# Kernel optimization log

Hardware: AMD Instinct MI355X
Metric: run time of the kernel (lower is better)

## Reference

```python
import jax, jax.numpy as jnp
import numpy as np

GLYPH_DIM = 4096
PADDING_IDX = GLYPH_DIM  # 4096
GLYPH_EMB = 20           # CHAR_EMB 16 + COLOR_EMB 4
HIDDEN = 32
MAX_LEN = 64


def setup_inputs() -> dict:
    key = jax.random.key(0)
    k1, k2, k3, k4, k5, k6, k7 = jax.random.split(key, 7)
    B, H, W = 8192, 21, 79
    glyph_chars = jax.random.randint(k1, (B, H, W), 0, 256, dtype=jnp.int32)
    glyph_colors = jax.random.randint(k2, (B, H, W), 0, 16, dtype=jnp.int32)
    # Embedding table with zero padding row (torch padding_idx semantics)
    emb_table = jax.random.normal(k3, (GLYPH_DIM + 1, GLYPH_EMB), dtype=jnp.float32) * 0.02
    emb_table = emb_table.at[PADDING_IDX].set(0.0)
    s = 1.0 / np.sqrt(HIDDEN)
    W_ih = jax.random.uniform(k4, (HIDDEN, GLYPH_EMB), minval=-s, maxval=s, dtype=jnp.float32)
    W_hh = jax.random.uniform(k5, (HIDDEN, HIDDEN), minval=-s, maxval=s, dtype=jnp.float32)
    b_ih = jax.random.uniform(k6, (HIDDEN,), minval=-s, maxval=s, dtype=jnp.float32)
    b_hh = jax.random.uniform(k7, (HIDDEN,), minval=-s, maxval=s, dtype=jnp.float32)
    return {"glyph_chars": glyph_chars, "glyph_colors": glyph_colors,
            "emb_table": emb_table, "W_ih": W_ih, "W_hh": W_hh,
            "b_ih": b_ih, "b_hh": b_hh}


def _encode_bag(glyph_chars, glyph_colors):
    """Batched sorted-unique compaction over the bounded glyph id range."""
    B = glyph_chars.shape[0]
    g_ids = ((glyph_chars << 4) + glyph_colors).reshape(B, -1)  # [B, H*W]
    # presence[b, g] = glyph g appears in sample b (batched histogram)
    bidx = jnp.broadcast_to(jnp.arange(B, dtype=g_ids.dtype)[:, None], g_ids.shape)
    presence = jnp.zeros((B, GLYPH_DIM), dtype=bool).at[bidx, g_ids].set(True)
    # compact: present ids keep their value, absent become PADDING_IDX (=4096),
    # so sorting yields ascending unique ids followed by padding.
    ids = jnp.arange(GLYPH_DIM, dtype=jnp.int32)
    keys = jnp.where(presence, ids, jnp.int32(PADDING_IDX))
    bag = jnp.sort(keys, axis=1)[:, :MAX_LEN]  # [B, MAX_LEN]
    lengths = jnp.minimum(presence.sum(axis=1), MAX_LEN)  # [B]
    return bag, lengths


def reference(glyph_chars, glyph_colors, emb_table, W_ih, W_hh, b_ih, b_hh):
    bag, lengths = _encode_bag(glyph_chars, glyph_colors)
    emb = emb_table[bag]  # [B, MAX_LEN, GLYPH_EMB]
    B = emb.shape[0]

    # packed RNN == plain RNN where hidden state freezes past each sequence length
    xs = jnp.swapaxes(emb, 0, 1)  # [T, B, E]

    def step(h, inp):
        xt, t = inp
        h_new = jnp.tanh(xt @ W_ih.T + b_ih + h @ W_hh.T + b_hh)
        h = jnp.where((t < lengths)[:, None], h_new, h)
        return h, None

    h0 = jnp.zeros((B, HIDDEN), dtype=emb.dtype)
    h, _ = jax.lax.scan(step, h0, (xs, jnp.arange(MAX_LEN)))
    return (h, emb, bag)
```

## Files before the change

### kernel.cpp

```cpp
#include <hip/hip_runtime.h>

#define HW 1659
#define PADID 4096
#define EMB 20
#define HID 32
#define MAXLEN 64

typedef float v2f __attribute__((ext_vector_type(2)));

template <int CTRL>
__device__ __forceinline__ float dppf(float v) {
    return __builtin_bit_cast(float,
        __builtin_amdgcn_update_dpp(0, __builtin_bit_cast(int, v),
                                    CTRL, 0xF, 0xF, true));
}
#define DPP_XOR1 0xB1
#define DPP_XOR2 0x4E
#define DPP_XOR7 0x141
#define DPP_XORF 0x140

__global__ __launch_bounds__(128) void proj_kernel(
    const float* __restrict__ emb_table, const float* __restrict__ W_ih,
    float* __restrict__ proj)
{
    const int tid = threadIdx.x;
    const int g = blockIdx.x * 4 + (tid >> 5);
    const int j = tid & 31;
    if (g > PADID) return;
    const float* er = emb_table + (size_t)g * EMB;
    const float* wr = W_ih + j * EMB;
    float s = 0.f;
#pragma unroll
    for (int k = 0; k < EMB; k++) s += wr[k] * er[k];
    proj[(size_t)g * HID + j] = s;
}

__global__ __launch_bounds__(256) void bag_emb_kernel(
    const int* __restrict__ chars, const int* __restrict__ colors,
    const float* __restrict__ emb_table,
    float* __restrict__ out_emb, float* __restrict__ out_bag)
{
    __shared__ unsigned char pres[4096];
    __shared__ int bagl[64];
    __shared__ int wsum[4];

    const int b   = blockIdx.x;
    const int tid = threadIdx.x;
    const int lane = tid & 63;
    const int wv   = tid >> 6;

    const int base = b * HW;
    const int pe = (4 - (base & 3)) & 3;
    const int nv = (HW - pe) >> 2;
    const int nt = HW - pe - (nv << 2);
    const int4* c4 = (const int4*)(chars + base + pe);
    const int4* k4 = (const int4*)(colors + base + pe);

    int4 ca = c4[tid], ka = k4[tid];
    const bool has2 = (tid + 256) < nv;
    const int i2 = has2 ? tid + 256 : tid;
    int4 cb = c4[i2], kb = k4[i2];
    int gp = -1, gt = -1;
    if (tid < pe) gp = (chars[base + tid] << 4) + colors[base + tid];
    if (tid < nt) {
        int i = base + pe + (nv << 2) + tid;
        gt = (chars[i] << 4) + colors[i];
    }

    ((uint4*)pres)[tid] = make_uint4(0u, 0u, 0u, 0u);
    if (tid < 64) bagl[tid] = PADID;
    __syncthreads();

    pres[(ca.x << 4) + ka.x] = 1;
    pres[(ca.y << 4) + ka.y] = 1;
    pres[(ca.z << 4) + ka.z] = 1;
    pres[(ca.w << 4) + ka.w] = 1;
    if (has2) {
        pres[(cb.x << 4) + kb.x] = 1;
        pres[(cb.y << 4) + kb.y] = 1;
        pres[(cb.z << 4) + kb.z] = 1;
        pres[(cb.w << 4) + kb.w] = 1;
    }
    if (gp >= 0) pres[gp] = 1;
    if (gt >= 0) pres[gt] = 1;
    __syncthreads();

    uint4 w4 = ((const uint4*)pres)[tid];
    const unsigned M = 0x01010101u;
    int cnt = __popc(w4.x & M) + __popc(w4.y & M)
            + __popc(w4.z & M) + __popc(w4.w & M);

    int pre = cnt;
#pragma unroll
    for (int d = 1; d < 64; d <<= 1) {
        int v = __shfl_up(pre, d, 64);
        if (lane >= d) pre += v;
    }
    if (lane == 63) wsum[wv] = pre;
    __syncthreads();
    int wbase = 0;
#pragma unroll
    for (int w2 = 0; w2 < 4; w2++) wbase += (w2 < wv) ? wsum[w2] : 0;
    int p = wbase + pre - cnt;

    unsigned wrd[4] = {w4.x, w4.y, w4.z, w4.w};
#pragma unroll
    for (int c = 0; c < 4; c++) {
#pragma unroll
        for (int k = 0; k < 4; k++) {
            if ((wrd[c] >> (8 * k)) & 1) {
                if (p < 64) bagl[p] = 16 * tid + 4 * c + k;
                p++;
            }
        }
    }
    __syncthreads();

    if (tid < 64) out_bag[(size_t)b * 64 + tid] = (float)bagl[tid];

    const float4* tab4 = (const float4*)emb_table;
    float4* dst4 = (float4*)(out_emb + (size_t)b * (MAXLEN * EMB));
    for (int q = tid; q < MAXLEN * 5; q += 256) {
        int t = q / 5;
        int m = q - t * 5;
        int row = bagl[t];
        dst4[q] = tab4[row * 5 + m];
    }
}

__global__ __launch_bounds__(128, 2) void rnn_kernel(
    const float* __restrict__ proj, const float* __restrict__ bagf,
    const float* __restrict__ W_hh,
    const float* __restrict__ b_ih, const float* __restrict__ b_hh,
    float* __restrict__ out_h)
{
    const int tid  = threadIdx.x;
    const int wv   = tid >> 6;
    const int lane = tid & 63;
    const int sl   = lane >> 4;
    const int ib   = wv * 4 + sl;
    const int jj   = lane & 15;
    const int b    = blockIdx.x * 8 + ib;

    const int GMAP[16] = {0,1,2,3, 7,6,5,4, 15,14,13,12,11,10,9,8};

    v2f w0[16], w1[16];
    const float2* wr0 = (const float2*)(W_hh + (2 * jj) * HID);
    const float2* wr1 = (const float2*)(W_hh + (2 * jj + 1) * HID);
#pragma unroll
    for (int m = 0; m < 16; m++) {
        const int c = jj ^ GMAP[m];
        float2 a = wr0[c], bb = wr1[c];
        w0[m] = (v2f){a.x, a.y};
        w1[m] = (v2f){bb.x, bb.y};
    }
    const float sb0 = b_ih[2 * jj]     + b_hh[2 * jj];
    const float sb1 = b_ih[2 * jj + 1] + b_hh[2 * jj + 1];

    const float* bps = bagf + (size_t)b * 64;

    unsigned long long mm0 = __ballot(bps[jj]      < 4095.5f);
    unsigned long long mm1 = __ballot(bps[jj + 16] < 4095.5f);
    unsigned long long mm2 = __ballot(bps[jj + 32] < 4095.5f);
    unsigned long long mm3 = __ballot(bps[jj + 48] < 4095.5f);
    const int sh = sl * 16;
    const int len = __popc((unsigned)((mm0 >> sh) & 0xFFFFu))
                  + __popc((unsigned)((mm1 >> sh) & 0xFFFFu))
                  + __popc((unsigned)((mm2 >> sh) & 0xFFFFu))
                  + __popc((unsigned)((mm3 >> sh) & 0xFFFFu));

    int idxC = (int)bps[1];
    float2 pv = ((const float2*)(proj + (size_t)((int)bps[0]) * HID))[jj];

    float h0 = 0.f, h1 = 0.f;
    for (int t = 0; t < MAXLEN; t++) {
        const int t2 = (t + 2 < MAXLEN) ? (t + 2) : (MAXLEN - 1);
        const int idxD = (int)bps[t2];
        const float2 pvn = ((const float2*)(proj + (size_t)idxC * HID))[jj];

        v2f g[16];
        g[0] = (v2f){h0, h1};
        g[1] = (v2f){dppf<DPP_XOR1>(g[0].x), dppf<DPP_XOR1>(g[0].y)};
        g[2] = (v2f){dppf<DPP_XOR2>(g[0].x), dppf<DPP_XOR2>(g[0].y)};
        g[3] = (v2f){dppf<DPP_XOR2>(g[1].x), dppf<DPP_XOR2>(g[1].y)};
#pragma unroll
        for (int m = 0; m < 4; m++)
            g[4 + m] = (v2f){dppf<DPP_XOR7>(g[m].x), dppf<DPP_XOR7>(g[m].y)};
#pragma unroll
        for (int m = 0; m < 8; m++)
            g[8 + m] = (v2f){dppf<DPP_XORF>(g[m].x), dppf<DPP_XORF>(g[m].y)};

        v2f a0 = (v2f){0.f, 0.f}, b0 = a0, a1 = a0, b1 = a0;
#pragma unroll
        for (int m = 0; m < 16; m += 2) {
            a0 = __builtin_elementwise_fma(w0[m],     g[m],     a0);
            b0 = __builtin_elementwise_fma(w0[m + 1], g[m + 1], b0);
            a1 = __builtin_elementwise_fma(w1[m],     g[m],     a1);
            b1 = __builtin_elementwise_fma(w1[m + 1], g[m + 1], b1);
        }
        float s0 = sb0 + pv.x + (a0.x + a0.y) + (b0.x + b0.y);
        float s1 = sb1 + pv.y + (a1.x + a1.y) + (b1.x + b1.y);

        float e0 = __expf(2.f * s0);
        float e1 = __expf(2.f * s1);
        float th0 = 1.f - 2.f * __builtin_amdgcn_rcpf(e0 + 1.f);
        float th1 = 1.f - 2.f * __builtin_amdgcn_rcpf(e1 + 1.f);

        h0 = (t < len) ? th0 : h0;
        h1 = (t < len) ? th1 : h1;

        pv = pvn; idxC = idxD;
    }

    ((float2*)(out_h + (size_t)b * HID))[jj] = make_float2(h0, h1);
}

__global__ __launch_bounds__(128, 4) void rnn_kernel_noproj(
    const float* __restrict__ emb, const float* __restrict__ bagf,
    const float* __restrict__ W_ih, const float* __restrict__ W_hh,
    const float* __restrict__ b_ih, const float* __restrict__ b_hh,
    float* __restrict__ out_h)
{
    __shared__ float hbuf[4][32];
    const int tid = threadIdx.x;
    const int ib  = tid >> 5;
    const int j   = tid & 31;
    const int b   = blockIdx.x * 4 + ib;

    float wih[EMB];
#pragma unroll
    for (int k = 0; k < EMB; k++) wih[k] = W_ih[j * EMB + k];
    float whh[HID];
#pragma unroll
    for (int k = 0; k < HID; k++) whh[k] = W_hh[j * HID + k];
    const float sbias = b_ih[j] + b_hh[j];

    const float* bp = bagf + (size_t)b * 64;
    unsigned long long m0 = __ballot(bp[j]      < 4095.5f);
    unsigned long long m1 = __ballot(bp[32 + j] < 4095.5f);
    const int half = ib & 1;
    const int len = __popc((unsigned)(m0 >> (half * 32)))
                  + __popc((unsigned)(m1 >> (half * 32)));

    hbuf[ib][j] = 0.f;
    asm volatile("s_waitcnt lgkmcnt(0)" ::: "memory");

    float h = 0.f;
    const float* xb = emb + (size_t)b * (MAXLEN * EMB);
    for (int t = 0; t < MAXLEN; t++) {
        const float4* xp = (const float4*)(xb + t * EMB);
        float4 x0 = xp[0], x1 = xp[1], x2 = xp[2], x3 = xp[3], x4 = xp[4];
        float s = sbias;
        const float4* hb4 = (const float4*)hbuf[ib];
#pragma unroll
        for (int m = 0; m < 8; m++) {
            float4 hv = hb4[m];
            s += whh[4*m+0]*hv.x + whh[4*m+1]*hv.y
               + whh[4*m+2]*hv.z + whh[4*m+3]*hv.w;
        }
        s += wih[0]*x0.x + wih[1]*x0.y + wih[2]*x0.z + wih[3]*x0.w;
        s += wih[4]*x1.x + wih[5]*x1.y + wih[6]*x1.z + wih[7]*x1.w;
        s += wih[8]*x2.x + wih[9]*x2.y + wih[10]*x2.z + wih[11]*x2.w;
        s += wih[12]*x3.x + wih[13]*x3.y + wih[14]*x3.z + wih[15]*x3.w;
        s += wih[16]*x4.x + wih[17]*x4.y + wih[18]*x4.z + wih[19]*x4.w;
        s = fminf(fmaxf(s, -9.f), 9.f);
        float e = __expf(2.f * s);
        float th = (e - 1.f) * __builtin_amdgcn_rcpf(e + 1.f);
        h = (t < len) ? th : h;
        hbuf[ib][j] = h;
        asm volatile("s_waitcnt lgkmcnt(0)" ::: "memory");
    }
    out_h[(size_t)b * HID + j] = h;
}

extern "C" void kernel_launch(void* const* d_in, const int* in_sizes, int n_in,
                              void* d_out, int out_size, void* d_ws, size_t ws_size,
                              hipStream_t stream) {
    const int*   chars     = (const int*)d_in[0];
    const int*   colors    = (const int*)d_in[1];
    const float* emb_table = (const float*)d_in[2];
    const float* W_ih      = (const float*)d_in[3];
    const float* W_hh      = (const float*)d_in[4];
    const float* b_ih      = (const float*)d_in[5];
    const float* b_hh      = (const float*)d_in[6];

    const int B = in_sizes[0] / HW;

    float* out     = (float*)d_out;
    float* out_h   = out;
    float* out_emb = out + (size_t)B * HID;
    float* out_bag = out_emb + (size_t)B * MAXLEN * EMB;

    const size_t proj_bytes = (size_t)(PADID + 1) * HID * sizeof(float);

    bag_emb_kernel<<<B, 256, 0, stream>>>(chars, colors, emb_table, out_emb, out_bag);

    if (ws_size >= proj_bytes) {
        float* proj = (float*)d_ws;
        proj_kernel<<<(PADID + 1 + 3) / 4, 128, 0, stream>>>(emb_table, W_ih, proj);
        rnn_kernel<<<B / 8, 128, 0, stream>>>(proj, out_bag, W_hh, b_ih, b_hh, out_h);
    } else {
        rnn_kernel_noproj<<<B / 4, 128, 0, stream>>>(out_emb, out_bag, W_ih, W_hh,
                                                     b_ih, b_hh, out_h);
    }
}
```

Measured before the change: 183.0 us.

## Process two samples per block in bag kernel, overlapping second sample's loads

The bag/embedding kernel now handles two batch samples per block. The second sample's chars and colors loads are issued before the first sample's scan and compaction, and the presence buffer is cleared and reused. This aims to hide global load latency and amortize block setup, at the cost of more registers and extra barriers, plus half as many blocks. It assumes B is even.

```diff
diff --git a/kernel.cpp b/kernel.cpp
--- a/kernel.cpp
+++ b/kernel.cpp
@@ -41,55 +41,72 @@
     float* __restrict__ out_emb, float* __restrict__ out_bag)
 {
     __shared__ unsigned char pres[4096];
-    __shared__ int bagl[64];
+    __shared__ int bagl[2][64];
     __shared__ int wsum[4];
 
-    const int b   = blockIdx.x;
-    const int tid = threadIdx.x;
+    const int tid  = threadIdx.x;
     const int lane = tid & 63;
     const int wv   = tid >> 6;
-
-    const int base = b * HW;
-    const int pe = (4 - (base & 3)) & 3;
-    const int nv = (HW - pe) >> 2;
-    const int nt = HW - pe - (nv << 2);
-    const int4* c4 = (const int4*)(chars + base + pe);
-    const int4* k4 = (const int4*)(colors + base + pe);
-
-    int4 ca = c4[tid], ka = k4[tid];
-    const bool has2 = (tid + 256) < nv;
-    const int i2 = has2 ? tid + 256 : tid;
-    int4 cb = c4[i2], kb = k4[i2];
-    int gp = -1, gt = -1;
-    if (tid < pe) gp = (chars[base + tid] << 4) + colors[base + tid];
-    if (tid < nt) {
-        int i = base + pe + (nv << 2) + tid;
-        gt = (chars[i] << 4) + colors[i];
+    const int b0   = blockIdx.x * 2;
+
+    const int base0 = b0 * HW;
+    const int pe0 = (4 - (base0 & 3)) & 3;
+    const int nv0 = (HW - pe0) >> 2;
+    const int nt0 = HW - pe0 - (nv0 << 2);
+    const int4* c40 = (const int4*)(chars + base0 + pe0);
+    const int4* k40 = (const int4*)(colors + base0 + pe0);
+    int4 ca0 = c40[tid], ka0 = k40[tid];
+    const bool h20 = (tid + 256) < nv0;
+    const int i20 = h20 ? tid + 256 : tid;
+    int4 cb0 = c40[i20], kb0 = k40[i20];
+    int gp0 = -1, gt0 = -1;
+    if (tid < pe0) gp0 = (chars[base0 + tid] << 4) + colors[base0 + tid];
+    if (tid < nt0) {
+        int i = base0 + pe0 + (nv0 << 2) + tid;
+        gt0 = (chars[i] << 4) + colors[i];
     }
 
     ((uint4*)pres)[tid] = make_uint4(0u, 0u, 0u, 0u);
-    if (tid < 64) bagl[tid] = PADID;
-    __syncthreads();
-
-    pres[(ca.x << 4) + ka.x] = 1;
-    pres[(ca.y << 4) + ka.y] = 1;
-    pres[(ca.z << 4) + ka.z] = 1;
-    pres[(ca.w << 4) + ka.w] = 1;
-    if (has2) {
-        pres[(cb.x << 4) + kb.x] = 1;
-        pres[(cb.y << 4) + kb.y] = 1;
-        pres[(cb.z << 4) + kb.z] = 1;
-        pres[(cb.w << 4) + kb.w] = 1;
-    }
-    if (gp >= 0) pres[gp] = 1;
-    if (gt >= 0) pres[gt] = 1;
-    __syncthreads();
+    if (tid < 128) ((int*)bagl)[tid] = PADID;
+    __syncthreads();
+
+    pres[(ca0.x << 4) + ka0.x] = 1;
+    pres[(ca0.y << 4) + ka0.y] = 1;
+    pres[(ca0.z << 4) + ka0.z] = 1;
+    pres[(ca0.w << 4) + ka0.w] = 1;
+    if (h20) {
+        pres[(cb0.x << 4) + kb0.x] = 1;
+        pres[(cb0.y << 4) + kb0.y] = 1;
+        pres[(cb0.z << 4) + kb0.z] = 1;
+        pres[(cb0.w << 4) + kb0.w] = 1;
+    }
+    if (gp0 >= 0) pres[gp0] = 1;
+    if (gt0 >= 0) pres[gt0] = 1;
+
+    const int base1 = base0 + HW;
+    const int pe1 = (4 - (base1 & 3)) & 3;
+    const int nv1 = (HW - pe1) >> 2;
+    const int nt1 = HW - pe1 - (nv1 << 2);
+    const int4* c41 = (const int4*)(chars + base1 + pe1);
+    const int4* k41 = (const int4*)(colors + base1 + pe1);
+    int4 ca1 = c41[tid], ka1 = k41[tid];
+    const bool h21 = (tid + 256) < nv1;
+    const int i21 = h21 ? tid + 256 : tid;
+    int4 cb1 = c41[i21], kb1 = k41[i21];
+    int gp1 = -1, gt1 = -1;
+    if (tid < pe1) gp1 = (chars[base1 + tid] << 4) + colors[base1 + tid];
+    if (tid < nt1) {
+        int i = base1 + pe1 + (nv1 << 2) + tid;
+        gt1 = (chars[i] << 4) + colors[i];
+    }
+    __syncthreads();
+
+    const unsigned M = 0x01010101u;
 
     uint4 w4 = ((const uint4*)pres)[tid];
-    const unsigned M = 0x01010101u;
+    ((uint4*)pres)[tid] = make_uint4(0u, 0u, 0u, 0u);
     int cnt = __popc(w4.x & M) + __popc(w4.y & M)
             + __popc(w4.z & M) + __popc(w4.w & M);
-
     int pre = cnt;
 #pragma unroll
     for (int d = 1; d < 64; d <<= 1) {
@@ -102,29 +119,86 @@
 #pragma unroll
     for (int w2 = 0; w2 < 4; w2++) wbase += (w2 < wv) ? wsum[w2] : 0;
     int p = wbase + pre - cnt;
-
-    unsigned wrd[4] = {w4.x, w4.y, w4.z, w4.w};
-#pragma unroll
-    for (int c = 0; c < 4; c++) {
-#pragma unroll
-        for (int k = 0; k < 4; k++) {
-            if ((wrd[c] >> (8 * k)) & 1) {
-                if (p < 64) bagl[p] = 16 * tid + 4 * c + k;
-                p++;
+    {
+        unsigned wrd[4] = {w4.x, w4.y, w4.z, w4.w};
+#pragma unroll
+        for (int c = 0; c < 4; c++) {
+#pragma unroll
+            for (int k = 0; k < 4; k++) {
+                if ((wrd[c] >> (8 * k)) & 1) {
+                    if (p < 64) bagl[0][p] = 16 * tid + 4 * c + k;
+                    p++;
+                }
             }
         }
     }
     __syncthreads();
 
-    if (tid < 64) out_bag[(size_t)b * 64 + tid] = (float)bagl[tid];
-
+    pres[(ca1.x << 4) + ka1.x] = 1;
+    pres[(ca1.y << 4) + ka1.y] = 1;
+    pres[(ca1.z << 4) + ka1.z] = 1;
+    pres[(ca1.w << 4) + ka1.w] = 1;
+    if (h21) {
+        pres[(cb1.x << 4) + kb1.x] = 1;
+        pres[(cb1.y << 4) + kb1.y] = 1;
+        pres[(cb1.z << 4) + kb1.z] = 1;
+        pres[(cb1.w << 4) + kb1.w] = 1;
+    }
+    if (gp1 >= 0) pres[gp1] = 1;
+    if (gt1 >= 0) pres[gt1] = 1;
+
+    if (tid < 64) out_bag[(size_t)b0 * 64 + tid] = (float)bagl[0][tid];
     const float4* tab4 = (const float4*)emb_table;
-    float4* dst4 = (float4*)(out_emb + (size_t)b * (MAXLEN * EMB));
-    for (int q = tid; q < MAXLEN * 5; q += 256) {
-        int t = q / 5;
-        int m = q - t * 5;
-        int row = bagl[t];
-        dst4[q] = tab4[row * 5 + m];
+    {
+        float4* dst4 = (float4*)(out_emb + (size_t)b0 * (MAXLEN * EMB));
+        for (int q = tid; q < MAXLEN * 5; q += 256) {
+            int t = q / 5;
+            int m = q - t * 5;
+            int row = bagl[0][t];
+            dst4[q] = tab4[row * 5 + m];
+        }
+    }
+    __syncthreads();
+
+    uint4 w4b = ((const uint4*)pres)[tid];
+    int cntb = __popc(w4b.x & M) + __popc(w4b.y & M)
+             + __popc(w4b.z & M) + __popc(w4b.w & M);
+    int preb = cntb;
+#pragma unroll
+    for (int d = 1; d < 64; d <<= 1) {
+        int v = __shfl_up(preb, d, 64);
+        if (lane >= d) preb += v;
+    }
+    if (lane == 63) wsum[wv] = preb;
+    __syncthreads();
+    int wbaseb = 0;
+#pragma unroll
+    for (int w2 = 0; w2 < 4; w2++) wbaseb += (w2 < wv) ? wsum[w2] : 0;
+    int pb = wbaseb + preb - cntb;
+    {
+        unsigned wrd[4] = {w4b.x, w4b.y, w4b.z, w4b.w};
+#pragma unroll
+        for (int c = 0; c < 4; c++) {
+#pragma unroll
+            for (int k = 0; k < 4; k++) {
+                if ((wrd[c] >> (8 * k)) & 1) {
+                    if (pb < 64) bagl[1][pb] = 16 * tid + 4 * c + k;
+                    pb++;
+                }
+            }
+        }
+    }
+    __syncthreads();
+
+    if (tid < 64) out_bag[(size_t)(b0 + 1) * 64 + tid] = (float)bagl[1][tid];
+    {
+        float4* dst4 = (float4*)(out_emb + (size_t)(b0 + 1) * (MAXLEN * EMB));
+        for (int q = tid; q < MAXLEN * 5; q += 256) {
+            int t = q / 5;
+            int m = q - t * 5;
+            int row = bagl[1][t];
+            dst4[q] = tab4[row * 5 + m];
+        }
     }
 }
 
@@ -293,7 +367,7 @@
 
     const size_t proj_bytes = (size_t)(PADID + 1) * HID * sizeof(float);
 
-    bag_emb_kernel<<<B, 256, 0, stream>>>(chars, colors, emb_table, out_emb, out_bag);
+    bag_emb_kernel<<<B / 2, 256, 0, stream>>>(chars, colors, emb_table, out_emb, out_bag);
 
     if (ws_size >= proj_bytes) {
         float* proj = (float*)d_ws;
```

After: 190.0 us. 3.8% more time.

## Batch-prefetch projected inputs in two 32-step halves and fully unroll RNN loop

Applied to the files above, without the earlier changes.

The RNN kernel now loads all 32 bag indices and their projected input rows into registers up front for each half of the sequence, instead of prefetching one step two iterations ahead. Both 32-step halves are fully unrolled, and the length is computed from the loaded indices rather than with ballots. The aim is to issue all gather loads at once so their latency overlaps, taking memory latency off the serial recurrence. This raises register pressure, since 64 extra VGPRs are held for pvA/pvB, so occupancy is pinned with waves_per_eu(2,2).

```diff
diff --git a/kernel.cpp b/kernel.cpp
--- a/kernel.cpp
+++ b/kernel.cpp
@@ -128,7 +128,9 @@
     }
 }
 
-__global__ __launch_bounds__(128, 2) void rnn_kernel(
+__global__ __launch_bounds__(128)
+__attribute__((amdgpu_waves_per_eu(2, 2)))
+void rnn_kernel(
     const float* __restrict__ proj, const float* __restrict__ bagf,
     const float* __restrict__ W_hh,
     const float* __restrict__ b_ih, const float* __restrict__ b_hh,
@@ -158,26 +160,25 @@
     const float sb1 = b_ih[2 * jj + 1] + b_hh[2 * jj + 1];
 
     const float* bps = bagf + (size_t)b * 64;
-
-    unsigned long long mm0 = __ballot(bps[jj]      < 4095.5f);
-    unsigned long long mm1 = __ballot(bps[jj + 16] < 4095.5f);
-    unsigned long long mm2 = __ballot(bps[jj + 32] < 4095.5f);
-    unsigned long long mm3 = __ballot(bps[jj + 48] < 4095.5f);
-    const int sh = sl * 16;
-    const int len = __popc((unsigned)((mm0 >> sh) & 0xFFFFu))
-                  + __popc((unsigned)((mm1 >> sh) & 0xFFFFu))
-                  + __popc((unsigned)((mm2 >> sh) & 0xFFFFu))
-                  + __popc((unsigned)((mm3 >> sh) & 0xFFFFu));
-
-    int idxC = (int)bps[1];
-    float2 pv = ((const float2*)(proj + (size_t)((int)bps[0]) * HID))[jj];
+    const float2* proj2 = (const float2*)proj;
+
+    float2 pvA[32];
+    int lenA = 0;
+    {
+        int idx[32];
+#pragma unroll
+        for (int t = 0; t < 32; t++) idx[t] = (int)bps[t];
+#pragma unroll
+        for (int t = 0; t < 32; t++) {
+            lenA += (idx[t] < PADID) ? 1 : 0;
+            pvA[t] = proj2[idx[t] * 16 + jj];
+        }
+    }
 
     float h0 = 0.f, h1 = 0.f;
-    for (int t = 0; t < MAXLEN; t++) {
-        const int t2 = (t + 2 < MAXLEN) ? (t + 2) : (MAXLEN - 1);
-        const int idxD = (int)bps[t2];
-        const float2 pvn = ((const float2*)(proj + (size_t)idxC * HID))[jj];
-
+
+#pragma unroll
+    for (int t = 0; t < 32; t++) {
         v2f g[16];
         g[0] = (v2f){h0, h1};
         g[1] = (v2f){dppf<DPP_XOR1>(g[0].x), dppf<DPP_XOR1>(g[0].y)};
@@ -198,18 +199,65 @@
             a1 = __builtin_elementwise_fma(w1[m],     g[m],     a1);
             b1 = __builtin_elementwise_fma(w1[m + 1], g[m + 1], b1);
         }
-        float s0 = sb0 + pv.x + (a0.x + a0.y) + (b0.x + b0.y);
-        float s1 = sb1 + pv.y + (a1.x + a1.y) + (b1.x + b1.y);
+        float s0 = sb0 + pvA[t].x + (a0.x + a0.y) + (b0.x + b0.y);
+        float s1 = sb1 + pvA[t].y + (a1.x + a1.y) + (b1.x + b1.y);
 
         float e0 = __expf(2.f * s0);
         float e1 = __expf(2.f * s1);
         float th0 = 1.f - 2.f * __builtin_amdgcn_rcpf(e0 + 1.f);
         float th1 = 1.f - 2.f * __builtin_amdgcn_rcpf(e1 + 1.f);
 
+        h0 = (t < lenA) ? th0 : h0;
+        h1 = (t < lenA) ? th1 : h1;
+    }
+
+    float2 pvB[32];
+    int lenB = 0;
+    {
+        int idx[32];
+#pragma unroll
+        for (int t = 0; t < 32; t++) idx[t] = (int)bps[32 + t];
+#pragma unroll
+        for (int t = 0; t < 32; t++) {
+            lenB += (idx[t] < PADID) ? 1 : 0;
+            pvB[t] = proj2[idx[t] * 16 + jj];
+        }
+    }
+    const int len = lenA + lenB;
+
+#pragma unroll
+    for (int t2 = 0; t2 < 32; t2++) {
+        const int t = 32 + t2;
+        v2f g[16];
+        g[0] = (v2f){h0, h1};
+        g[1] = (v2f){dppf<DPP_XOR1>(g[0].x), dppf<DPP_XOR1>(g[0].y)};
+        g[2] = (v2f){dppf<DPP_XOR2>(g[0].x), dppf<DPP_XOR2>(g[0].y)};
+        g[3] = (v2f){dppf<DPP_XOR2>(g[1].x), dppf<DPP_XOR2>(g[1].y)};
+#pragma unroll
+        for (int m = 0; m < 4; m++)
+            g[4 + m] = (v2f){dppf<DPP_XOR7>(g[m].x), dppf<DPP_XOR7>(g[m].y)};
+#pragma unroll
+        for (int m = 0; m < 8; m++)
+            g[8 + m] = (v2f){dppf<DPP_XORF>(g[m].x), dppf<DPP_XORF>(g[m].y)};
+
+        v2f a0 = (v2f){0.f, 0.f}, b0 = a0, a1 = a0, b1 = a0;
+#pragma unroll
+        for (int m = 0; m < 16; m += 2) {
+            a0 = __builtin_elementwise_fma(w0[m],     g[m],     a0);
+            b0 = __builtin_elementwise_fma(w0[m + 1], g[m + 1], b0);
+            a1 = __builtin_elementwise_fma(w1[m],     g[m],     a1);
+            b1 = __builtin_elementwise_fma(w1[m + 1], g[m + 1], b1);
+        }
+        float s0 = sb0 + pvB[t2].x + (a0.x + a0.y) + (b0.x + b0.y);
+        float s1 = sb1 + pvB[t2].y + (a1.x + a1.y) + (b1.x + b1.y);
+
+        float e0 = __expf(2.f * s0);
+        float e1 = __expf(2.f * s1);
+        float th0 = 1.f - 2.f * __builtin_amdgcn_rcpf(e0 + 1.f);
+        float th1 = 1.f - 2.f * __builtin_amdgcn_rcpf(e1 + 1.f);
+
         h0 = (t < len) ? th0 : h0;
         h1 = (t < len) ? th1 : h1;
-
-        pv = pvn; idxC = idxD;
     }
 
     ((float2*)(out_h + (size_t)b * HID))[jj] = make_float2(h0, h1);
```

After: 181.2 us. About the same (-1.0%).

## Batch projection gathers in chunks of 16 steps and unroll RNN loop fully

Applied to the files above, without the earlier changes.

The RNN loop is restructured into four fully unrolled chunks. Each chunk first loads 16 bag indices and issues all 16 projection gathers, then runs the 16 recurrent steps. This replaces the depth-2 software prefetch with deeper memory-level parallelism. The ballot/popcount length computation is dropped in favour of a per-step padding test on the index, and occupancy is pinned to 2 waves per EU. The cost is higher register pressure from 16 buffered float2 values and indices, plus larger code.

```diff
diff --git a/kernel.cpp b/kernel.cpp
--- a/kernel.cpp
+++ b/kernel.cpp
@@ -128,7 +128,9 @@
     }
 }
 
-__global__ __launch_bounds__(128, 2) void rnn_kernel(
+__global__ __launch_bounds__(128)
+__attribute__((amdgpu_waves_per_eu(2, 2)))
+void rnn_kernel(
     const float* __restrict__ proj, const float* __restrict__ bagf,
     const float* __restrict__ W_hh,
     const float* __restrict__ b_ih, const float* __restrict__ b_hh,
@@ -158,58 +160,54 @@
     const float sb1 = b_ih[2 * jj + 1] + b_hh[2 * jj + 1];
 
     const float* bps = bagf + (size_t)b * 64;
-
-    unsigned long long mm0 = __ballot(bps[jj]      < 4095.5f);
-    unsigned long long mm1 = __ballot(bps[jj + 16] < 4095.5f);
-    unsigned long long mm2 = __ballot(bps[jj + 32] < 4095.5f);
-    unsigned long long mm3 = __ballot(bps[jj + 48] < 4095.5f);
-    const int sh = sl * 16;
-    const int len = __popc((unsigned)((mm0 >> sh) & 0xFFFFu))
-                  + __popc((unsigned)((mm1 >> sh) & 0xFFFFu))
-                  + __popc((unsigned)((mm2 >> sh) & 0xFFFFu))
-                  + __popc((unsigned)((mm3 >> sh) & 0xFFFFu));
-
-    int idxC = (int)bps[1];
-    float2 pv = ((const float2*)(proj + (size_t)((int)bps[0]) * HID))[jj];
+    const float2* proj2 = (const float2*)proj;
 
     float h0 = 0.f, h1 = 0.f;
-    for (int t = 0; t < MAXLEN; t++) {
-        const int t2 = (t + 2 < MAXLEN) ? (t + 2) : (MAXLEN - 1);
-        const int idxD = (int)bps[t2];
-        const float2 pvn = ((const float2*)(proj + (size_t)idxC * HID))[jj];
-
-        v2f g[16];
-        g[0] = (v2f){h0, h1};
-        g[1] = (v2f){dppf<DPP_XOR1>(g[0].x), dppf<DPP_XOR1>(g[0].y)};
-        g[2] = (v2f){dppf<DPP_XOR2>(g[0].x), dppf<DPP_XOR2>(g[0].y)};
-        g[3] = (v2f){dppf<DPP_XOR2>(g[1].x), dppf<DPP_XOR2>(g[1].y)};
-#pragma unroll
-        for (int m = 0; m < 4; m++)
-            g[4 + m] = (v2f){dppf<DPP_XOR7>(g[m].x), dppf<DPP_XOR7>(g[m].y)};
-#pragma unroll
-        for (int m = 0; m < 8; m++)
-            g[8 + m] = (v2f){dppf<DPP_XORF>(g[m].x), dppf<DPP_XORF>(g[m].y)};
-
-        v2f a0 = (v2f){0.f, 0.f}, b0 = a0, a1 = a0, b1 = a0;
-#pragma unroll
-        for (int m = 0; m < 16; m += 2) {
-            a0 = __builtin_elementwise_fma(w0[m],     g[m],     a0);
-            b0 = __builtin_elementwise_fma(w0[m + 1], g[m + 1], b0);
-            a1 = __builtin_elementwise_fma(w1[m],     g[m],     a1);
-            b1 = __builtin_elementwise_fma(w1[m + 1], g[m + 1], b1);
+
+#pragma unroll
+    for (int ch = 0; ch < 4; ch++) {
+        int idx[16];
+#pragma unroll
+        for (int i = 0; i < 16; i++) idx[i] = (int)bps[ch * 16 + i];
+        float2 pv[16];
+#pragma unroll
+        for (int i = 0; i < 16; i++) pv[i] = proj2[idx[i] * 16 + jj];
+
+#pragma unroll
+        for (int i = 0; i < 16; i++) {
+            const bool upd = idx[i] < PADID;
+
+            v2f g[16];
+            g[0] = (v2f){h0, h1};
+            g[1] = (v2f){dppf<DPP_XOR1>(g[0].x), dppf<DPP_XOR1>(g[0].y)};
+            g[2] = (v2f){dppf<DPP_XOR2>(g[0].x), dppf<DPP_XOR2>(g[0].y)};
+            g[3] = (v2f){dppf<DPP_XOR2>(g[1].x), dppf<DPP_XOR2>(g[1].y)};
+#pragma unroll
+            for (int m = 0; m < 4; m++)
+                g[4 + m] = (v2f){dppf<DPP_XOR7>(g[m].x), dppf<DPP_XOR7>(g[m].y)};
+#pragma unroll
+            for (int m = 0; m < 8; m++)
+                g[8 + m] = (v2f){dppf<DPP_XORF>(g[m].x), dppf<DPP_XORF>(g[m].y)};
+
+            v2f a0 = (v2f){0.f, 0.f}, b0 = a0, a1 = a0, b1 = a0;
+#pragma unroll
+            for (int m = 0; m < 16; m += 2) {
+                a0 = __builtin_elementwise_fma(w0[m],     g[m],     a0);
+                b0 = __builtin_elementwise_fma(w0[m + 1], g[m + 1], b0);
+                a1 = __builtin_elementwise_fma(w1[m],     g[m],     a1);
+                b1 = __builtin_elementwise_fma(w1[m + 1], g[m + 1], b1);
+            }
+            float s0 = sb0 + pv[i].x + (a0.x + a0.y) + (b0.x + b0.y);
+            float s1 = sb1 + pv[i].y + (a1.x + a1.y) + (b1.x + b1.y);
+
+            float e0 = __expf(2.f * s0);
+            float e1 = __expf(2.f * s1);
+            float th0 = 1.f - 2.f * __builtin_amdgcn_rcpf(e0 + 1.f);
+            float th1 = 1.f - 2.f * __builtin_amdgcn_rcpf(e1 + 1.f);
+
+            h0 = upd ? th0 : h0;
+            h1 = upd ? th1 : h1;
         }
-        float s0 = sb0 + pv.x + (a0.x + a0.y) + (b0.x + b0.y);
-        float s1 = sb1 + pv.y + (a1.x + a1.y) + (b1.x + b1.y);
-
-        float e0 = __expf(2.f * s0);
-        float e1 = __expf(2.f * s1);
-        float th0 = 1.f - 2.f * __builtin_amdgcn_rcpf(e0 + 1.f);
-        float th1 = 1.f - 2.f * __builtin_amdgcn_rcpf(e1 + 1.f);
-
-        h0 = (t < len) ? th0 : h0;
-        h1 = (t < len) ? th1 : h1;
-
-        pv = pvn; idxC = idxD;
     }
 
     ((float2*)(out_h + (size_t)b * HID))[jj] = make_float2(h0, h1);
```

Result: no change. 180.5 us (-1.4%).
